# Performance work log

Hardware: AMD Instinct MI355X
Metric: run time of the kernel (lower is better)

The kernel has to match this reference:

```python
import jax, jax.numpy as jnp
import numpy as np

HID, XD, ZD, K = 512, 128, 64, 3
B, T = 64, 1024

def setup_inputs() -> dict:
    key = jax.random.key(0)
    ks = jax.random.split(key, 10)
    s = lambda *d: 1.0 / np.sqrt(d[0])
    return {
        "x_seq": jax.random.normal(ks[0], (B, T, XD), jnp.float32),
        "conv_w": jax.random.normal(ks[1], (K, XD, HID), jnp.float32) * (1.0/np.sqrt(K*XD)),
        "conv_b": jnp.zeros((HID,), jnp.float32),
        "Wx": jax.random.normal(ks[2], (HID, 4*HID), jnp.float32) * (1.0/np.sqrt(HID)),
        "Wh": jax.random.normal(ks[3], (HID, 4*HID), jnp.float32) * (1.0/np.sqrt(HID)),
        "b": jnp.zeros((4*HID,), jnp.float32),
        "W1": jax.random.normal(ks[4], (HID, HID), jnp.float32) * (1.0/np.sqrt(HID)),
        "b1": jnp.zeros((HID,), jnp.float32),
        "W2": jax.random.normal(ks[5], (HID, 2*ZD), jnp.float32) * (1.0/np.sqrt(HID)),
        "b2": jnp.zeros((2*ZD,), jnp.float32),
    }

def _forward(x_seq, conv_w, conv_b, Wx, Wh, b, W1, b1, W2, b2):
    # Conv1D, SAME padding: (B, T, x_dim) -> (B, T, HID)
    conv = jax.lax.conv_general_dilated(
        x_seq, conv_w, window_strides=(1,), padding="SAME",
        dimension_numbers=("NWC", "WIO", "NWC")) + conv_b

    def step(carry, x_t):
        c, h = carry
        # flax LSTMCell: gates i,f,g,o; input dense (no bias) + hidden dense (bias)
        z = x_t @ Wx + h @ Wh + b  # (B, 4*HID)
        i, f, g, o = jnp.split(z, 4, axis=-1)
        i, f, o = jax.nn.sigmoid(i), jax.nn.sigmoid(f), jax.nn.sigmoid(o)
        g = jnp.tanh(g)
        c_new = f * c + i * g
        h_new = o * jnp.tanh(c_new)
        return (c_new, h_new), h_new

    c0 = jnp.zeros((conv.shape[0], HID), conv.dtype)
    h0 = jnp.zeros((conv.shape[0], HID), conv.dtype)
    _, h_seq = jax.lax.scan(step, (c0, h0), jnp.swapaxes(conv, 0, 1))  # (T, B, HID)
    h_seq = jnp.swapaxes(h_seq, 0, 1)  # (B, T, HID)

    # per-step 2-layer MLP head, applied vectorized over (B, T)
    x = jax.nn.relu(h_seq @ W1 + b1)
    out = x @ W2 + b2  # (B, T, 2*ZD)
    mu, log_sigma = jnp.split(out, 2, axis=-1)
    return mu, log_sigma

def reference(x_seq, conv_w, conv_b, Wx, Wh, b, W1, b1, W2, b2):
    return _forward(x_seq, conv_w, conv_b, Wx, Wh, b, W1, b1, W2, b2)
```

## Files before the change

kernel.cpp:

```cpp
#include <hip/hip_runtime.h>
#include <math.h>

typedef unsigned short u16;
typedef unsigned int   u32;
typedef unsigned long long u64;
typedef _Float16 f16;
typedef __attribute__((ext_vector_type(8))) _Float16 f16x8;
typedef __attribute__((ext_vector_type(4))) float    f32x4;
typedef __attribute__((ext_vector_type(4))) u32      u32x4;

#define T_SEQ 1024
#define NB    64
#define HID   512
#define KC    384
#define G4    2048
#define MR    (NB*T_SEQ)
#define ZD2   128

__device__ __align__(16) f16   g_xwin[(size_t)MR*KC];
__device__ __align__(16) f16   g_cwxt[(size_t)G4*KC];
__device__              float  g_bb[G4];
__device__ __align__(16) f16   g_whT[(size_t)G4*HID];
__device__ __align__(16) f16   g_w1T[(size_t)HID*HID];
__device__ __align__(16) f16   g_w2T[(size_t)ZD2*HID];
__device__              float  g_b1f[HID];
__device__              float  g_b2f[ZD2];
__device__ __align__(16) float g_XW[(size_t)MR*G4];
__device__ __align__(16) f16   g_hseq[(size_t)MR*HID];
__device__ __align__(16) f16   g_tmp1[(size_t)MR*HID];
__device__ __align__(16) u64   g_hstep[(size_t)(T_SEQ+1)*NB*128];
__device__              int    g_in_fp32;

__device__ inline float bf2f(u16 u){ union{u32 i; float f;} v; v.i = ((u32)u)<<16; return v.f; }
__device__ inline u16  f2bf(float f){ union{u32 i; float f;} v; v.f = f; u32 u = v.i;
                                      return (u16)((u + 0x7fffu + ((u>>16)&1u))>>16); }
__device__ inline float load_in(const void* p, size_t i){
  return g_in_fp32 ? ((const float*)p)[i] : bf2f(((const u16*)p)[i]);
}
__device__ inline float fsig(float x){
  return __builtin_amdgcn_rcpf(1.f + __builtin_amdgcn_exp2f(-1.44269504f*x));
}
__device__ inline float ftanh(float x){
  x = fminf(fmaxf(x, -10.f), 10.f);
  float e = __builtin_amdgcn_exp2f(2.88539008f*x);
  return (e - 1.f) * __builtin_amdgcn_rcpf(e + 1.f);
}

__global__ void k_probe(const void* x){
  __shared__ int cnt;
  if (threadIdx.x == 0) cnt = 0;
  __syncthreads();
  int loc = 0;
  for (int i = threadIdx.x; i < 4096; i += 256){
    float a = fabsf(bf2f(((const u16*)x)[i]));
    if (a > 0.01f && a < 10.f) loc++;
  }
  atomicAdd(&cnt, loc);
  __syncthreads();
  if (threadIdx.x == 0) g_in_fp32 = (cnt < 3276) ? 1 : 0;
}

__global__ void k_init(const void* b1, const void* b2){
  int i = blockIdx.x*256 + threadIdx.x;
  if (i < HID)        g_b1f[i] = load_in(b1, i);
  if (i < ZD2)        g_b2f[i] = load_in(b2, i);
  if (i < NB*128)     g_hstep[i] = 0ULL;
}

__global__ void k_fill(){
  size_t i = (size_t)blockIdx.x*256 + threadIdx.x;
  u64* p = g_hstep + (size_t)NB*128;
  const size_t n = (size_t)T_SEQ*NB*128;
  for (size_t j = i; j < n; j += (size_t)4096*256) p[j] = ~0ULL;
}

__global__ void k_combine(const void* conv_w, const void* conv_b, const void* Wx, const void* b){
  int j  = blockIdx.x*256 + threadIdx.x;
  int kc = blockIdx.y;
  float acc = 0.f;
  if (kc < KC){
    for (int m = 0; m < HID; ++m)
      acc += load_in(conv_w, (size_t)kc*HID + m) * load_in(Wx, (size_t)m*G4 + j);
    g_cwxt[(size_t)j*KC + kc] = (f16)acc;
  } else {
    for (int m = 0; m < HID; ++m)
      acc += load_in(conv_b, m) * load_in(Wx, (size_t)m*G4 + j);
    g_bb[j] = acc + load_in(b, j);
  }
}

__device__ inline void trans_body(const void* src, f16* dst, int R, int C){
  size_t i = (size_t)blockIdx.x*256 + threadIdx.x;
  if (i >= (size_t)R*C) return;
  int c = (int)(i / (size_t)R), r = (int)(i % (size_t)R);
  dst[i] = (f16)load_in(src, (size_t)r*C + c);
}
__global__ void k_trans_wh(const void* Wh){ trans_body(Wh, g_whT, HID, G4); }
__global__ void k_trans_w1(const void* W1){ trans_body(W1, g_w1T, HID, HID); }
__global__ void k_trans_w2(const void* W2){ trans_body(W2, g_w2T, HID, ZD2); }

__global__ void k_xwin(const void* x){
  size_t i = (size_t)blockIdx.x*256 + threadIdx.x;
  if (i >= (size_t)MR*KC) return;
  int row = (int)(i / KC), kc = (int)(i % KC);
  int k = kc >> 7, c = kc & 127;
  int b = row >> 10, t = row & 1023;
  int ts = t - 1 + k;
  float v = 0.f;
  if (ts >= 0 && ts < T_SEQ) v = load_in(x, ((size_t)b*T_SEQ + ts)*128 + c);
  g_xwin[i] = (f16)v;
}

template<int MODE, int K>
__device__ inline void gemm_body(const f16* __restrict__ A, const f16* __restrict__ BT,
                                 const float* __restrict__ bias, void* __restrict__ C, int N){
  const int tid = threadIdx.x;
  const int w = tid >> 6, lane = tid & 63;
  const int q = lane >> 4, ln = lane & 15;
  const int n0 = blockIdx.x * 128;
  const int m0 = blockIdx.y * 64;
  const f16* ap = A + (size_t)(m0 + w*16 + ln)*K + q*8;
  const f16* bp = BT + (size_t)(n0 + ln)*K + q*8;
  f32x4 acc[8] = {};
  #pragma unroll 4
  for (int k = 0; k < K; k += 32){
    f16x8 af = *(const f16x8*)(ap + k);
    #pragma unroll
    for (int nt = 0; nt < 8; ++nt){
      f16x8 bf = *(const f16x8*)(bp + (size_t)nt*16*K + k);
      acc[nt] = __builtin_amdgcn_mfma_f32_16x16x32_f16(af, bf, acc[nt], 0, 0, 0);
    }
  }
  const int f32o = g_in_fp32;
  #pragma unroll
  for (int nt = 0; nt < 8; ++nt){
    const int col = n0 + nt*16 + ln;
    const float bv = bias[col];
    #pragma unroll
    for (int r = 0; r < 4; ++r){
      const int row = m0 + w*16 + q*4 + r;
      float v = acc[nt][r] + bv;
      if (MODE == 0){
        ((float*)C)[(size_t)row*N + col] = v;
      } else if (MODE == 1){
        ((f16*)C)[(size_t)row*N + col] = (f16)fmaxf(v, 0.f);
      } else {
        size_t idx = (col < 64) ? ((size_t)row*64 + col)
                                : (4194304UL + (size_t)row*64 + (size_t)(col - 64));
        if (f32o) ((float*)C)[idx] = v;
        else      ((u16*)C)[idx]   = f2bf(v);
      }
    }
  }
}
__global__ __launch_bounds__(256) void k_gemm_xw(){   gemm_body<0,KC >(g_xwin, g_cwxt, g_bb,  g_XW,   G4 ); }
__global__ __launch_bounds__(256) void k_gemm_mlp1(){ gemm_body<1,HID>(g_hseq, g_w1T,  g_b1f, g_tmp1, HID); }
__global__ __launch_bounds__(256) void k_gemm_mlp2(void* out){ gemm_body<2,HID>(g_tmp1, g_w2T, g_b2f, out, ZD2); }

__global__ __launch_bounds__(256, 1) void k_lstm(){
  const int g   = blockIdx.x;
  const int tid = threadIdx.x;
  const int w = tid >> 6, lane = tid & 63;
  const int q = lane >> 4, ln = lane & 15;
  const int  c8 = ln & 7;
  const bool lo = ln < 8;
  const int  zc0  = (lo ? 0 : HID)       + g*8 + c8;
  const int  zc1  = (lo ? 2*HID : 3*HID) + g*8 + c8;
  const int  colh = g*8 + c8;
  const int  am   = w*16 + ln;

  const size_t zA = (size_t)((ln>>3)*HID     + g*8 + c8) * HID;
  const size_t zB = (size_t)((2+(ln>>3))*HID + g*8 + c8) * HID;
  f16x8 bf0[16], bf1[16];
  #pragma unroll
  for (int kk = 0; kk < 16; ++kk){
    bf0[kk] = *(const f16x8*)&g_whT[zA + kk*32 + q*8];
    bf1[kk] = *(const f16x8*)&g_whT[zB + kk*32 + q*8];
  }

  float c_st[4] = {0.f, 0.f, 0.f, 0.f};

  size_t rowb[4];
  #pragma unroll
  for (int r = 0; r < 4; ++r) rowb[r] = (size_t)(w*16 + q*4 + r)*T_SEQ*G4;
  float xwa[4], xwb[4];
  #pragma unroll
  for (int r = 0; r < 4; ++r){
    xwa[r] = g_XW[rowb[r] + zc0];
    xwb[r] = g_XW[rowb[r] + zc1];
  }

  u64 addr = (u64)(const void*)(g_hstep + ((size_t)am)*128 + (size_t)q*2);

  for (int t = 0; t < T_SEQ; ++t){
    u32x4 hr[16];
    for (;;){
      asm volatile(
        "global_load_dwordx4 %0, %16, off sc0 sc1\n"
        "global_load_dwordx4 %1, %16, off offset:64 sc0 sc1\n"
        "global_load_dwordx4 %2, %16, off offset:128 sc0 sc1\n"
        "global_load_dwordx4 %3, %16, off offset:192 sc0 sc1\n"
        "global_load_dwordx4 %4, %16, off offset:256 sc0 sc1\n"
        "global_load_dwordx4 %5, %16, off offset:320 sc0 sc1\n"
        "global_load_dwordx4 %6, %16, off offset:384 sc0 sc1\n"
        "global_load_dwordx4 %7, %16, off offset:448 sc0 sc1\n"
        "global_load_dwordx4 %8, %16, off offset:512 sc0 sc1\n"
        "global_load_dwordx4 %9, %16, off offset:576 sc0 sc1\n"
        "global_load_dwordx4 %10, %16, off offset:640 sc0 sc1\n"
        "global_load_dwordx4 %11, %16, off offset:704 sc0 sc1\n"
        "global_load_dwordx4 %12, %16, off offset:768 sc0 sc1\n"
        "global_load_dwordx4 %13, %16, off offset:832 sc0 sc1\n"
        "global_load_dwordx4 %14, %16, off offset:896 sc0 sc1\n"
        "global_load_dwordx4 %15, %16, off offset:960 sc0 sc1\n"
        "s_waitcnt vmcnt(0)"
        : "=&v"(hr[0]),  "=&v"(hr[1]),  "=&v"(hr[2]),  "=&v"(hr[3]),
          "=&v"(hr[4]),  "=&v"(hr[5]),  "=&v"(hr[6]),  "=&v"(hr[7]),
          "=&v"(hr[8]),  "=&v"(hr[9]),  "=&v"(hr[10]), "=&v"(hr[11]),
          "=&v"(hr[12]), "=&v"(hr[13]), "=&v"(hr[14]), "=&v"(hr[15])
        : "v"(addr)
        : "memory");
      u32 bad = 0;
      #pragma unroll
      for (int i = 0; i < 16; ++i){
        bad |= (u32)((hr[i].x & hr[i].y) == 0xFFFFFFFFu);
        bad |= (u32)((hr[i].z & hr[i].w) == 0xFFFFFFFFu);
      }
      if (!__any((int)bad)) break;
      __builtin_amdgcn_s_sleep(1);
    }
    addr += (u64)NB*128*8;

    const int tn = (t+1 < T_SEQ) ? (t+1) : t;
    float xna[4], xnb[4];
    #pragma unroll
    for (int r = 0; r < 4; ++r){
      const size_t base = rowb[r] + (size_t)tn*G4;
      xna[r] = g_XW[base + zc0];
      xnb[r] = g_XW[base + zc1];
    }

    f32x4 a0a = {0.f,0.f,0.f,0.f}, a0b = {0.f,0.f,0.f,0.f};
    f32x4 a1a = {0.f,0.f,0.f,0.f}, a1b = {0.f,0.f,0.f,0.f};
    #pragma unroll
    for (int kk = 0; kk < 16; ++kk){
      f16x8 af = __builtin_bit_cast(f16x8, hr[kk]);
      if (kk & 1){
        a0b = __builtin_amdgcn_mfma_f32_16x16x32_f16(af, bf0[kk], a0b, 0, 0, 0);
        a1b = __builtin_amdgcn_mfma_f32_16x16x32_f16(af, bf1[kk], a1b, 0, 0, 0);
      } else {
        a0a = __builtin_amdgcn_mfma_f32_16x16x32_f16(af, bf0[kk], a0a, 0, 0, 0);
        a1a = __builtin_amdgcn_mfma_f32_16x16x32_f16(af, bf1[kk], a1a, 0, 0, 0);
      }
    }
    f32x4 a0 = a0a + a0b;
    f32x4 a1 = a1a + a1b;

    f16 h16v[4];
    #pragma unroll
    for (int r = 0; r < 4; ++r){
      float z0 = a0[r] + xwa[r];
      float z1 = a1[r] + xwb[r];
      float zf = __shfl_xor(z0, 8, 64);
      float zo = __shfl_xor(z1, 8, 64);
      float iv = fsig(z0);
      float fv = fsig(zf);
      float gv = ftanh(z1);
      float ov = fsig(zo);
      float cn = fv*c_st[r] + iv*gv;
      c_st[r] = cn;
      float hvf = ov*ftanh(cn);
      f16 h16 = (f16)hvf;
      h16v[r] = h16;
      u32 me = (u32)__builtin_bit_cast(u16, h16);
      u32 p1 = me | (((u32)__shfl_xor((int)me, 1, 64)) << 16);
      u32 p2 = (u32)__shfl_xor((int)p1, 2, 64);
      u64 pk = (u64)p1 | ((u64)p2 << 32);
      if (lo && (c8 & 3) == 0){
        int m = w*16 + q*4 + r;
        __hip_atomic_store(g_hstep + ((size_t)(t+1)*NB + m)*128 + (size_t)g*2 + (c8>>2),
                           pk, __ATOMIC_RELAXED, __HIP_MEMORY_SCOPE_AGENT);
      }
    }
    if (lo){
      #pragma unroll
      for (int r = 0; r < 4; ++r){
        int m = w*16 + q*4 + r;
        g_hseq[((size_t)m*T_SEQ + t)*HID + colh] = h16v[r];
      }
    }
    #pragma unroll
    for (int r = 0; r < 4; ++r){ xwa[r] = xna[r]; xwb[r] = xnb[r]; }
  }
}

extern "C" void kernel_launch(void* const* d_in, const int* in_sizes, int n_in,
                              void* d_out, int out_size, void* d_ws, size_t ws_size,
                              hipStream_t stream){
  const void* x      = d_in[0];
  const void* conv_w = d_in[1];
  const void* conv_b = d_in[2];
  const void* Wx     = d_in[3];
  const void* Wh     = d_in[4];
  const void* b      = d_in[5];
  const void* W1     = d_in[6];
  const void* b1     = d_in[7];
  const void* W2     = d_in[8];
  const void* b2     = d_in[9];
  (void)in_sizes; (void)n_in; (void)out_size; (void)d_ws; (void)ws_size;

  hipLaunchKernelGGL(k_probe,   dim3(1),        dim3(256), 0, stream, x);
  hipLaunchKernelGGL(k_init,    dim3(256),      dim3(256), 0, stream, b1, b2);
  hipLaunchKernelGGL(k_fill,    dim3(4096),     dim3(256), 0, stream);
  hipLaunchKernelGGL(k_combine, dim3(8, 385),   dim3(256), 0, stream, conv_w, conv_b, Wx, b);
  hipLaunchKernelGGL(k_trans_wh,dim3(4096),     dim3(256), 0, stream, Wh);
  hipLaunchKernelGGL(k_trans_w1,dim3(1024),     dim3(256), 0, stream, W1);
  hipLaunchKernelGGL(k_trans_w2,dim3(256),      dim3(256), 0, stream, W2);
  hipLaunchKernelGGL(k_xwin,    dim3(98304),    dim3(256), 0, stream, x);
  hipLaunchKernelGGL(k_gemm_xw, dim3(16, 1024), dim3(256), 0, stream);
  hipLaunchKernelGGL(k_lstm,    dim3(64),       dim3(256), 0, stream);
  hipLaunchKernelGGL(k_gemm_mlp1, dim3(4, 1024), dim3(256), 0, stream);
  hipLaunchKernelGGL(k_gemm_mlp2, dim3(1, 1024), dim3(256), 0, stream, d_out);
}
```

Before: 8.156 ms.

## Stream h slices with per-slice waits and move recurrent weights to LDS

The recurrent weight slice moves from per-thread registers into a padded shared-memory tile that is re-read every step. The per-step h fetch now waits on each 16-byte slice separately, using decreasing vmcnt counts, so MFMAs can start as soon as each slice arrives instead of after all loads finish. Sentinel polling is done per slice, and the next step's XW values are prefetched through inline asm with precomputed pointers. The aim is to overlap load latency with compute on the serial recurrence and to free VGPRs, at the cost of LDS reads on the critical path and reliance on in-order vmcnt accounting.

```diff
diff --git a/kernel.cpp b/kernel.cpp
--- a/kernel.cpp
+++ b/kernel.cpp
@@ -16,6 +16,7 @@
 #define G4    2048
 #define MR    (NB*T_SEQ)
 #define ZD2   128
+#define WPAD  528
 
 __device__ __align__(16) f16   g_xwin[(size_t)MR*KC];
 __device__ __align__(16) f16   g_cwxt[(size_t)G4*KC];
@@ -44,6 +45,9 @@
   x = fminf(fmaxf(x, -10.f), 10.f);
   float e = __builtin_amdgcn_exp2f(2.88539008f*x);
   return (e - 1.f) * __builtin_amdgcn_rcpf(e + 1.f);
+}
+__device__ inline int slice_ok(u32x4 v){
+  return !(((v.x & v.y) == 0xFFFFFFFFu) | ((v.z & v.w) == 0xFFFFFFFFu));
 }
 
 __global__ void k_probe(const void* x){
@@ -158,6 +162,7 @@
 __global__ __launch_bounds__(256) void k_gemm_mlp2(void* out){ gemm_body<2,HID>(g_tmp1, g_w2T, g_b2f, out, ZD2); }
 
 __global__ __launch_bounds__(256, 1) void k_lstm(){
+  __shared__ __align__(16) f16 whs[32*WPAD];
   const int g   = blockIdx.x;
   const int tid = threadIdx.x;
   const int w = tid >> 6, lane = tid & 63;
@@ -169,14 +174,12 @@
   const int  colh = g*8 + c8;
   const int  am   = w*16 + ln;
 
-  const size_t zA = (size_t)((ln>>3)*HID     + g*8 + c8) * HID;
-  const size_t zB = (size_t)((2+(ln>>3))*HID + g*8 + c8) * HID;
-  f16x8 bf0[16], bf1[16];
-  #pragma unroll
-  for (int kk = 0; kk < 16; ++kk){
-    bf0[kk] = *(const f16x8*)&g_whT[zA + kk*32 + q*8];
-    bf1[kk] = *(const f16x8*)&g_whT[zB + kk*32 + q*8];
-  }
+  for (int idx = tid; idx < 32*HID; idx += 256){
+    int r = idx >> 9, k = idx & 511;
+    int zcol = (r >> 3)*HID + g*8 + (r & 7);
+    whs[r*WPAD + k] = g_whT[(size_t)zcol*HID + k];
+  }
+  __syncthreads();
 
   float c_st[4] = {0.f, 0.f, 0.f, 0.f};
 
@@ -189,69 +192,105 @@
     xwa[r] = g_XW[rowb[r] + zc0];
     xwb[r] = g_XW[rowb[r] + zc1];
   }
+  asm volatile("s_waitcnt vmcnt(0)"
+    : "+v"(xwa[0]), "+v"(xwa[1]), "+v"(xwa[2]), "+v"(xwa[3]),
+      "+v"(xwb[0]), "+v"(xwb[1]), "+v"(xwb[2]), "+v"(xwb[3]) :: "memory");
+  u64 pxa[4], pxb[4];
+  #pragma unroll
+  for (int r = 0; r < 4; ++r){
+    pxa[r] = (u64)(const void*)&g_XW[rowb[r] + (size_t)G4 + zc0];
+    pxb[r] = (u64)(const void*)&g_XW[rowb[r] + (size_t)G4 + zc1];
+  }
 
   u64 addr = (u64)(const void*)(g_hstep + ((size_t)am)*128 + (size_t)q*2);
 
+  #pragma unroll 1
   for (int t = 0; t < T_SEQ; ++t){
     u32x4 hr[16];
-    for (;;){
-      asm volatile(
-        "global_load_dwordx4 %0, %16, off sc0 sc1\n"
-        "global_load_dwordx4 %1, %16, off offset:64 sc0 sc1\n"
-        "global_load_dwordx4 %2, %16, off offset:128 sc0 sc1\n"
-        "global_load_dwordx4 %3, %16, off offset:192 sc0 sc1\n"
-        "global_load_dwordx4 %4, %16, off offset:256 sc0 sc1\n"
-        "global_load_dwordx4 %5, %16, off offset:320 sc0 sc1\n"
-        "global_load_dwordx4 %6, %16, off offset:384 sc0 sc1\n"
-        "global_load_dwordx4 %7, %16, off offset:448 sc0 sc1\n"
-        "global_load_dwordx4 %8, %16, off offset:512 sc0 sc1\n"
-        "global_load_dwordx4 %9, %16, off offset:576 sc0 sc1\n"
-        "global_load_dwordx4 %10, %16, off offset:640 sc0 sc1\n"
-        "global_load_dwordx4 %11, %16, off offset:704 sc0 sc1\n"
-        "global_load_dwordx4 %12, %16, off offset:768 sc0 sc1\n"
-        "global_load_dwordx4 %13, %16, off offset:832 sc0 sc1\n"
-        "global_load_dwordx4 %14, %16, off offset:896 sc0 sc1\n"
-        "global_load_dwordx4 %15, %16, off offset:960 sc0 sc1\n"
-        "s_waitcnt vmcnt(0)"
-        : "=&v"(hr[0]),  "=&v"(hr[1]),  "=&v"(hr[2]),  "=&v"(hr[3]),
-          "=&v"(hr[4]),  "=&v"(hr[5]),  "=&v"(hr[6]),  "=&v"(hr[7]),
-          "=&v"(hr[8]),  "=&v"(hr[9]),  "=&v"(hr[10]), "=&v"(hr[11]),
-          "=&v"(hr[12]), "=&v"(hr[13]), "=&v"(hr[14]), "=&v"(hr[15])
-        : "v"(addr)
-        : "memory");
-      u32 bad = 0;
-      #pragma unroll
-      for (int i = 0; i < 16; ++i){
-        bad |= (u32)((hr[i].x & hr[i].y) == 0xFFFFFFFFu);
-        bad |= (u32)((hr[i].z & hr[i].w) == 0xFFFFFFFFu);
-      }
-      if (!__any((int)bad)) break;
-      __builtin_amdgcn_s_sleep(1);
-    }
-    addr += (u64)NB*128*8;
-
-    const int tn = (t+1 < T_SEQ) ? (t+1) : t;
-    float xna[4], xnb[4];
-    #pragma unroll
-    for (int r = 0; r < 4; ++r){
-      const size_t base = rowb[r] + (size_t)tn*G4;
-      xna[r] = g_XW[base + zc0];
-      xnb[r] = g_XW[base + zc1];
-    }
+    asm volatile(
+      "global_load_dwordx4 %0, %16, off sc0 sc1\n"
+      "global_load_dwordx4 %1, %16, off offset:64 sc0 sc1\n"
+      "global_load_dwordx4 %2, %16, off offset:128 sc0 sc1\n"
+      "global_load_dwordx4 %3, %16, off offset:192 sc0 sc1\n"
+      "global_load_dwordx4 %4, %16, off offset:256 sc0 sc1\n"
+      "global_load_dwordx4 %5, %16, off offset:320 sc0 sc1\n"
+      "global_load_dwordx4 %6, %16, off offset:384 sc0 sc1\n"
+      "global_load_dwordx4 %7, %16, off offset:448 sc0 sc1\n"
+      "global_load_dwordx4 %8, %16, off offset:512 sc0 sc1\n"
+      "global_load_dwordx4 %9, %16, off offset:576 sc0 sc1\n"
+      "global_load_dwordx4 %10, %16, off offset:640 sc0 sc1\n"
+      "global_load_dwordx4 %11, %16, off offset:704 sc0 sc1\n"
+      "global_load_dwordx4 %12, %16, off offset:768 sc0 sc1\n"
+      "global_load_dwordx4 %13, %16, off offset:832 sc0 sc1\n"
+      "global_load_dwordx4 %14, %16, off offset:896 sc0 sc1\n"
+      "global_load_dwordx4 %15, %16, off offset:960 sc0 sc1"
+      : "=&v"(hr[0]),  "=&v"(hr[1]),  "=&v"(hr[2]),  "=&v"(hr[3]),
+        "=&v"(hr[4]),  "=&v"(hr[5]),  "=&v"(hr[6]),  "=&v"(hr[7]),
+        "=&v"(hr[8]),  "=&v"(hr[9]),  "=&v"(hr[10]), "=&v"(hr[11]),
+        "=&v"(hr[12]), "=&v"(hr[13]), "=&v"(hr[14]), "=&v"(hr[15])
+      : "v"(addr)
+      : "memory");
+    float xn0,xn1,xn2,xn3,xn4,xn5,xn6,xn7;
+    asm volatile(
+      "global_load_dword %0, %8, off\n"
+      "global_load_dword %1, %9, off\n"
+      "global_load_dword %2, %10, off\n"
+      "global_load_dword %3, %11, off\n"
+      "global_load_dword %4, %12, off\n"
+      "global_load_dword %5, %13, off\n"
+      "global_load_dword %6, %14, off\n"
+      "global_load_dword %7, %15, off"
+      : "=&v"(xn0), "=&v"(xn1), "=&v"(xn2), "=&v"(xn3),
+        "=&v"(xn4), "=&v"(xn5), "=&v"(xn6), "=&v"(xn7)
+      : "v"(pxa[0]), "v"(pxa[1]), "v"(pxa[2]), "v"(pxa[3]),
+        "v"(pxb[0]), "v"(pxb[1]), "v"(pxb[2]), "v"(pxb[3])
+      : "memory");
 
     f32x4 a0a = {0.f,0.f,0.f,0.f}, a0b = {0.f,0.f,0.f,0.f};
     f32x4 a1a = {0.f,0.f,0.f,0.f}, a1b = {0.f,0.f,0.f,0.f};
-    #pragma unroll
-    for (int kk = 0; kk < 16; ++kk){
-      f16x8 af = __builtin_bit_cast(f16x8, hr[kk]);
-      if (kk & 1){
-        a0b = __builtin_amdgcn_mfma_f32_16x16x32_f16(af, bf0[kk], a0b, 0, 0, 0);
-        a1b = __builtin_amdgcn_mfma_f32_16x16x32_f16(af, bf1[kk], a1b, 0, 0, 0);
-      } else {
-        a0a = __builtin_amdgcn_mfma_f32_16x16x32_f16(af, bf0[kk], a0a, 0, 0, 0);
-        a1a = __builtin_amdgcn_mfma_f32_16x16x32_f16(af, bf1[kk], a1a, 0, 0, 0);
-      }
-    }
+
+#define H_SLICE(KK, NSTR, OFFSTR)                                              \
+    {                                                                          \
+      asm volatile("s_waitcnt vmcnt(" NSTR ")"                                 \
+                   : "+v"(hr[KK]) :: "memory");                                \
+      while (!__all(slice_ok(hr[KK]))){                                        \
+        asm volatile("global_load_dwordx4 %0, %1, off offset:" OFFSTR          \
+                     " sc0 sc1\n\ts_waitcnt vmcnt(0)"                          \
+                     : "=&v"(hr[KK]) : "v"(addr) : "memory");                  \
+      }                                                                        \
+      f16x8 af = __builtin_bit_cast(f16x8, hr[KK]);                            \
+      f16x8 b0 = *(const f16x8*)&whs[(     ln)*WPAD + (KK)*32 + q*8];          \
+      f16x8 b1 = *(const f16x8*)&whs[(16 + ln)*WPAD + (KK)*32 + q*8];          \
+      if ((KK) & 1){                                                           \
+        a0b = __builtin_amdgcn_mfma_f32_16x16x32_f16(af, b0, a0b, 0, 0, 0);    \
+        a1b = __builtin_amdgcn_mfma_f32_16x16x32_f16(af, b1, a1b, 0, 0, 0);    \
+      } else {                                                                 \
+        a0a = __builtin_amdgcn_mfma_f32_16x16x32_f16(af, b0, a0a, 0, 0, 0);    \
+        a1a = __builtin_amdgcn_mfma_f32_16x16x32_f16(af, b1, a1a, 0, 0, 0);    \
+      }                                                                        \
+    }
+    H_SLICE(0,  "23", "0")
+    H_SLICE(1,  "22", "64")
+    H_SLICE(2,  "21", "128")
+    H_SLICE(3,  "20", "192")
+    H_SLICE(4,  "19", "256")
+    H_SLICE(5,  "18", "320")
+    H_SLICE(6,  "17", "384")
+    H_SLICE(7,  "16", "448")
+    H_SLICE(8,  "15", "512")
+    H_SLICE(9,  "14", "576")
+    H_SLICE(10, "13", "640")
+    H_SLICE(11, "12", "704")
+    H_SLICE(12, "11", "768")
+    H_SLICE(13, "10", "832")
+    H_SLICE(14, "9",  "896")
+    H_SLICE(15, "8",  "960")
+#undef H_SLICE
+
+    asm volatile("s_waitcnt vmcnt(0)"
+      : "+v"(xn0), "+v"(xn1), "+v"(xn2), "+v"(xn3),
+        "+v"(xn4), "+v"(xn5), "+v"(xn6), "+v"(xn7) :: "memory");
+
     f32x4 a0 = a0a + a0b;
     f32x4 a1 = a1a + a1b;
 
@@ -288,8 +327,13 @@
         g_hseq[((size_t)m*T_SEQ + t)*HID + colh] = h16v[r];
       }
     }
-    #pragma unroll
-    for (int r = 0; r < 4; ++r){ xwa[r] = xna[r]; xwb[r] = xnb[r]; }
+    xwa[0]=xn0; xwa[1]=xn1; xwa[2]=xn2; xwa[3]=xn3;
+    xwb[0]=xn4; xwb[1]=xn5; xwb[2]=xn6; xwb[3]=xn7;
+    if (t < T_SEQ-2){
+      #pragma unroll
+      for (int r = 0; r < 4; ++r){ pxa[r] += (u64)G4*4; pxb[r] += (u64)G4*4; }
+    }
+    addr += (u64)NB*128*8;
   }
 }
 
```

Measured after the change: 13.60 ms. 66.8% more time.
